# Optimization experiments

Hardware: AMD Instinct MI355X
Metric: run time of the kernel (lower is better)

The kernel has to match this reference:

```python
import jax, jax.numpy as jnp
import numpy as np

IN_FEATURES = 512
OUT_FEATURES = 512
GRID_MIN = -2.0
GRID_MAX = 2.0
NUM_GRIDS = 8
SPLINE_SCALE = 0.1
BATCH = 16384


def setup_inputs() -> dict:
    key = jax.random.key(0)
    kx, kw = jax.random.split(key)
    x = jax.random.normal(kx, (BATCH, IN_FEATURES), dtype=jnp.float32)
    grid = jnp.linspace(GRID_MIN, GRID_MAX, NUM_GRIDS, dtype=jnp.float32)
    spline_weight = (
        jax.random.normal(kw, (IN_FEATURES * NUM_GRIDS, OUT_FEATURES), dtype=jnp.float32)
        * SPLINE_SCALE
    )
    return {"x": x, "grid": grid, "spline_weight": spline_weight}


def reference(x, grid, spline_weight):
    # denominator h = (grid_max - grid_min) / (num_grids - 1)
    h = (GRID_MAX - GRID_MIN) / (NUM_GRIDS - 1)
    # basis: [B, in_features, num_grids]
    basis = jnp.exp(-jnp.square((x[..., None] - grid) / h))
    # flatten to [B, in_features * num_grids] and GEMM
    return basis.reshape(basis.shape[0], -1) @ spline_weight
```

## Files before the change

### kernel.cpp

```cpp
#include <hip/hip_runtime.h>
#include <hip/hip_bf16.h>

#define BATCH 16384
#define IN_F 512
#define OUT_F 512
#define NG 8
#define KTOT (IN_F * NG)

#define SH    2.1019642153762872f
#define SSTEP 1.2011224087864498f
#define BC0N  4.2039284307525745f
#define RC1   2.4022448175728996f
#define RC2  -1.4426950408889634f
#define RQ    0.13533528323661270f

typedef __attribute__((ext_vector_type(8))) short short8;
typedef __attribute__((ext_vector_type(4))) float f32x4;
typedef __attribute__((ext_vector_type(2))) float f32x2;
typedef __attribute__((ext_vector_type(4))) unsigned int u32x4;
typedef __attribute__((ext_vector_type(2))) unsigned int u32x2;

__device__ __forceinline__ unsigned fbits(float f) {
    union { float f; unsigned u; } v; v.f = f; return v.u;
}
__device__ __forceinline__ unsigned pack2bf(float lo, float hi) {
    unsigned a = (fbits(lo) + 0x8000u) >> 16;
    unsigned b = (fbits(hi) + 0x8000u) & 0xFFFF0000u;
    return a | b;
}

__device__ __forceinline__ void lds_barrier() {
    __asm__ volatile("" ::: "memory");
    __builtin_amdgcn_sched_barrier(0);
    __builtin_amdgcn_s_waitcnt(0xC07F);
    __builtin_amdgcn_s_barrier();
    __builtin_amdgcn_sched_barrier(0);
    __asm__ volatile("" ::: "memory");
}

__global__ void wt_swizzle(const float* __restrict__ W, unsigned short* __restrict__ Wt) {
    const int gid  = blockIdx.x * 256 + threadIdx.x;
    const int lane = gid & 63;
    const int f    = (gid >> 6) & 7;
    const int kt   = (gid >> 9) & 63;
    const int s    = gid >> 15;
    const int j  = f & 3, kk = f >> 2;
    const int l15 = lane & 15, lq = lane >> 4;
    const int n  = s * 64 + j * 16 + l15;
    const int k0 = kt * 64 + kk * 32 + lq * 8;
    u32x4 pk;
#pragma unroll
    for (int e = 0; e < 4; ++e)
        pk[e] = pack2bf(W[(size_t)(k0 + 2 * e) * OUT_F + n],
                        W[(size_t)(k0 + 2 * e + 1) * OUT_F + n]);
    *(u32x4*)(Wt + (size_t)gid * 8) = pk;
}

__global__ __launch_bounds__(256, 2) void gauss_gemm5(
        const float* __restrict__ X, const unsigned short* __restrict__ Wt,
        float* __restrict__ Out) {
    __shared__ __align__(16) unsigned short sA[2 * 64 * 64];

    const int tid  = threadIdx.x;
    const int lane = tid & 63;
    const int wave = tid >> 6;
    const int cb = blockIdx.x & 1;
    const int rb = blockIdx.x >> 1;
    const int m0 = rb * 64;
    const int n0 = cb * 256;
    const int l15 = lane & 15;
    const int lq  = lane >> 4;
    const int s   = cb * 4 + wave;

    const int aw0 = lane * 64 + (((2 * wave)     ^ (lane & 7)) << 3);
    const int aw1 = lane * 64 + (((2 * wave + 1) ^ (lane & 7)) << 3);
    const float* xlp = X + (size_t)(m0 + lane) * IN_F + wave * 2;

    int aofs[2][4];
#pragma unroll
    for (int kk = 0; kk < 2; ++kk)
#pragma unroll
        for (int i = 0; i < 4; ++i)
            aofs[kk][i] = (i * 16 + l15) * 64 + (((kk * 4 + lq) ^ (l15 & 7)) << 3);

    const unsigned short* bptr = Wt + (size_t)s * 262144 + lane * 8;

    f32x4 acc[4][4];
#pragma unroll
    for (int i = 0; i < 4; ++i)
#pragma unroll
        for (int j = 0; j < 4; ++j)
            acc[i][j] = (f32x4){0.f, 0.f, 0.f, 0.f};

    auto stageA = [&](f32x2 xv, int buf) {
        unsigned short* base = sA + buf * 4096;
#pragma unroll
        for (int h = 0; h < 2; ++h) {
            const float t0 = fmaf(h ? xv.y : xv.x, SH, BC0N);
            float r = __builtin_amdgcn_exp2f(fmaf(t0, RC1, RC2));
            const float v0 = __builtin_amdgcn_exp2f(-t0 * t0);
            const float v1 = v0 * r;
            r *= RQ; const float v2 = v1 * r;
            r *= RQ; const float v3 = v2 * r;
            r *= RQ; const float v4 = v3 * r;
            r *= RQ; const float v5 = v4 * r;
            r *= RQ; const float v6 = v5 * r;
            r *= RQ; const float v7 = v6 * r;
            u32x4 pk;
            pk[0] = pack2bf(v0, v1);
            pk[1] = pack2bf(v2, v3);
            pk[2] = pack2bf(v4, v5);
            pk[3] = pack2bf(v6, v7);
            *(u32x4*)(base + (h ? aw1 : aw0)) = pk;
        }
    };

    short8 bfA[8], bfB[8];
    f32x2 xr;

    {
        f32x2 x0 = *(const f32x2*)(xlp);
        stageA(x0, 0);
#pragma unroll
        for (int f = 0; f < 8; ++f)
            bfA[f] = *(const short8*)(bptr + f * 512);
        xr = *(const f32x2*)(xlp + 8);
        lds_barrier();
    }

#define GG_ITER(KT, BUF, BU, BF)                                               \
    {                                                                          \
        const int kn1 = ((KT) + 1 < 63) ? (KT) + 1 : 63;                       \
        const int kn2 = ((KT) + 2 < 63) ? (KT) + 2 : 63;                       \
        short8 af[2][4];                                                       \
        _Pragma("unroll")                                                      \
        for (int kk = 0; kk < 2; ++kk)                                         \
            _Pragma("unroll")                                                  \
            for (int i = 0; i < 4; ++i)                                        \
                af[kk][i] = *(const short8*)(sA + (BUF) * 4096 + aofs[kk][i]); \
        _Pragma("unroll")                                                      \
        for (int f = 0; f < 8; ++f)                                            \
            BF[f] = *(const short8*)(bptr + (size_t)kn1 * 4096 + f * 512);     \
        stageA(xr, (BUF) ^ 1);                                                 \
        xr = *(const f32x2*)(xlp + (size_t)kn2 * 8);                           \
        _Pragma("unroll")                                                      \
        for (int kk = 0; kk < 2; ++kk)                                         \
            _Pragma("unroll")                                                  \
            for (int i = 0; i < 4; ++i)                                        \
                _Pragma("unroll")                                              \
                for (int j = 0; j < 4; ++j)                                    \
                    acc[i][j] = __builtin_amdgcn_mfma_f32_16x16x32_bf16(       \
                        af[kk][i], BU[kk * 4 + j], acc[i][j], 0, 0, 0);        \
        lds_barrier();                                                         \
    }

    for (int kt = 0; kt < 64; kt += 2) {
        GG_ITER(kt,     0, bfA, bfB)
        GG_ITER(kt + 1, 1, bfB, bfA)
    }
#undef GG_ITER

#pragma unroll
    for (int i = 0; i < 4; ++i) {
        const int r0 = m0 + i * 16 + lq * 4;
#pragma unroll
        for (int j = 0; j < 4; ++j) {
            const int c = n0 + wave * 64 + j * 16 + l15;
#pragma unroll
            for (int e = 0; e < 4; ++e)
                Out[(size_t)(r0 + e) * OUT_F + c] = acc[i][j][e];
        }
    }
}

#define BM 128
#define BN 128
#define BK 64
#define LDA 72
#define LDB 72

__global__ __launch_bounds__(256, 2) void gauss_gemm_fb(
        const float* __restrict__ X, const float* __restrict__ W,
        float* __restrict__ Out) {
    __shared__ __align__(16) unsigned short sA[BM * LDA];
    __shared__ __align__(16) unsigned short sB2[BN * LDB];

    const int tid  = threadIdx.x;
    const int lane = tid & 63;
    const int wave = tid >> 6;
    const int rb = blockIdx.x >> 2;
    const int cbx = blockIdx.x & 3;
    const int m0 = rb * BM;
    const int n0 = cbx * BN;
    const int wr = (wave >> 1) * 64;
    const int wc = (wave & 1) * 64;
    const int l15 = lane & 15;
    const int lq  = lane >> 4;

    f32x4 acc[4][4];
#pragma unroll
    for (int i = 0; i < 4; ++i)
#pragma unroll
        for (int j = 0; j < 4; ++j)
            acc[i][j] = (f32x4){0.f, 0.f, 0.f, 0.f};

    const int arow = tid & 127;
    const int axq  = tid >> 7;

    for (int kt = 0; kt < KTOT / BK; ++kt) {
        const int k0  = kt * BK;
        const int xc0 = kt * (BK / NG);

        const f32x4 xv = *(const f32x4*)(X + (size_t)(m0 + arow) * IN_F + xc0 + 4 * axq);
        unsigned short* sArow = sA + arow * LDA + axq * 32;
#pragma unroll
        for (int j = 0; j < 4; ++j) {
            const float xs = xv[j] * SH;
            u32x4 pk;
#pragma unroll
            for (int g = 0; g < 8; g += 2) {
                float t0 = xs + (BC0N - g * SSTEP);
                float t1 = xs + (BC0N - (g + 1) * SSTEP);
                unsigned u0 = fbits(__builtin_amdgcn_exp2f(-t0 * t0)) + 0x8000u;
                unsigned u1 = fbits(__builtin_amdgcn_exp2f(-t1 * t1)) + 0x8000u;
                pk[g >> 1] = (u0 >> 16) | (u1 & 0xFFFF0000u);
            }
            *(u32x4*)(sArow + j * 8) = pk;
        }

#pragma unroll
        for (int p = 0; p < 8; ++p) {
            int id = p * 256 + tid;
            int n  = id & 127;
            int k4 = id >> 7;
            const float* wp = W + (size_t)(k0 + k4 * 4) * OUT_F + n0 + n;
            u32x2 v;
            v[0] = pack2bf(wp[0], wp[OUT_F]);
            v[1] = pack2bf(wp[2 * OUT_F], wp[3 * OUT_F]);
            *(u32x2*)(sB2 + n * LDB + k4 * 4) = v;
        }

        __syncthreads();

#pragma unroll
        for (int kk = 0; kk < BK; kk += 32) {
            short8 af[4], bfv[4];
#pragma unroll
            for (int i = 0; i < 4; ++i)
                af[i] = *(const short8*)(sA + (wr + i * 16 + l15) * LDA + kk + lq * 8);
#pragma unroll
            for (int i = 0; i < 4; ++i)
                bfv[i] = *(const short8*)(sB2 + (wc + i * 16 + l15) * LDB + kk + lq * 8);
#pragma unroll
            for (int i = 0; i < 4; ++i)
#pragma unroll
                for (int j = 0; j < 4; ++j)
                    acc[i][j] = __builtin_amdgcn_mfma_f32_16x16x32_bf16(af[i], bfv[j], acc[i][j], 0, 0, 0);
        }

        __syncthreads();
    }

#pragma unroll
    for (int i = 0; i < 4; ++i) {
        const int r0 = m0 + wr + i * 16 + lq * 4;
#pragma unroll
        for (int j = 0; j < 4; ++j) {
            const int c = n0 + wc + j * 16 + l15;
#pragma unroll
            for (int e = 0; e < 4; ++e)
                Out[(size_t)(r0 + e) * OUT_F + c] = acc[i][j][e];
        }
    }
}

extern "C" void kernel_launch(void* const* d_in, const int* in_sizes, int n_in,
                              void* d_out, int out_size, void* d_ws, size_t ws_size,
                              hipStream_t stream) {
    (void)in_sizes; (void)n_in; (void)out_size;
    const float* X = (const float*)d_in[0];
    const float* W = (const float*)d_in[2];
    float* Out = (float*)d_out;

    const size_t wt_bytes = (size_t)KTOT * OUT_F * sizeof(unsigned short);
    if (ws_size >= wt_bytes) {
        unsigned short* Wt = (unsigned short*)d_ws;
        wt_swizzle<<<dim3(KTOT * OUT_F / 8 / 256), 256, 0, stream>>>(W, Wt);
        gauss_gemm5<<<dim3((BATCH / 64) * (OUT_F / 256)), 256, 0, stream>>>(X, Wt, Out);
    } else {
        gauss_gemm_fb<<<dim3((BATCH / BM) * (OUT_F / BN)), 256, 0, stream>>>(X, W, Out);
    }
}
```

Baseline: 156.2 us.

## Compute Gaussian basis directly in MFMA A-fragment registers, drop LDS staging

```diff
diff --git a/kernel.cpp b/kernel.cpp
--- a/kernel.cpp
+++ b/kernel.cpp
@@ -27,15 +27,6 @@
     unsigned a = (fbits(lo) + 0x8000u) >> 16;
     unsigned b = (fbits(hi) + 0x8000u) & 0xFFFF0000u;
     return a | b;
-}
-
-__device__ __forceinline__ void lds_barrier() {
-    __asm__ volatile("" ::: "memory");
-    __builtin_amdgcn_sched_barrier(0);
-    __builtin_amdgcn_s_waitcnt(0xC07F);
-    __builtin_amdgcn_s_barrier();
-    __builtin_amdgcn_sched_barrier(0);
-    __asm__ volatile("" ::: "memory");
 }
 
 __global__ void wt_swizzle(const float* __restrict__ W, unsigned short* __restrict__ Wt) {
@@ -47,7 +38,7 @@
     const int j  = f & 3, kk = f >> 2;
     const int l15 = lane & 15, lq = lane >> 4;
     const int n  = s * 64 + j * 16 + l15;
-    const int k0 = kt * 64 + kk * 32 + lq * 8;
+    const int k0 = kt * 64 + (lq * 2 + kk) * 8;
     u32x4 pk;
 #pragma unroll
     for (int e = 0; e < 4; ++e)
@@ -56,11 +47,9 @@
     *(u32x4*)(Wt + (size_t)gid * 8) = pk;
 }
 
-__global__ __launch_bounds__(256, 2) void gauss_gemm5(
+__global__ __launch_bounds__(256, 2) void gauss_gemm6(
         const float* __restrict__ X, const unsigned short* __restrict__ Wt,
         float* __restrict__ Out) {
-    __shared__ __align__(16) unsigned short sA[2 * 64 * 64];
-
     const int tid  = threadIdx.x;
     const int lane = tid & 63;
     const int wave = tid >> 6;
@@ -72,18 +61,12 @@
     const int lq  = lane >> 4;
     const int s   = cb * 4 + wave;
 
-    const int aw0 = lane * 64 + (((2 * wave)     ^ (lane & 7)) << 3);
-    const int aw1 = lane * 64 + (((2 * wave + 1) ^ (lane & 7)) << 3);
-    const float* xlp = X + (size_t)(m0 + lane) * IN_F + wave * 2;
-
-    int aofs[2][4];
-#pragma unroll
-    for (int kk = 0; kk < 2; ++kk)
-#pragma unroll
-        for (int i = 0; i < 4; ++i)
-            aofs[kk][i] = (i * 16 + l15) * 64 + (((kk * 4 + lq) ^ (l15 & 7)) << 3);
-
     const unsigned short* bptr = Wt + (size_t)s * 262144 + lane * 8;
+
+    const float* xrow[4];
+#pragma unroll
+    for (int i = 0; i < 4; ++i)
+        xrow[i] = X + (size_t)(m0 + i * 16 + l15) * IN_F + lq * 2;
 
     f32x4 acc[4][4];
 #pragma unroll
@@ -92,71 +75,62 @@
         for (int j = 0; j < 4; ++j)
             acc[i][j] = (f32x4){0.f, 0.f, 0.f, 0.f};
 
-    auto stageA = [&](f32x2 xv, int buf) {
-        unsigned short* base = sA + buf * 4096;
-#pragma unroll
-        for (int h = 0; h < 2; ++h) {
-            const float t0 = fmaf(h ? xv.y : xv.x, SH, BC0N);
-            float r = __builtin_amdgcn_exp2f(fmaf(t0, RC1, RC2));
-            const float v0 = __builtin_amdgcn_exp2f(-t0 * t0);
-            const float v1 = v0 * r;
-            r *= RQ; const float v2 = v1 * r;
-            r *= RQ; const float v3 = v2 * r;
-            r *= RQ; const float v4 = v3 * r;
-            r *= RQ; const float v5 = v4 * r;
-            r *= RQ; const float v6 = v5 * r;
-            r *= RQ; const float v7 = v6 * r;
-            u32x4 pk;
-            pk[0] = pack2bf(v0, v1);
-            pk[1] = pack2bf(v2, v3);
-            pk[2] = pack2bf(v4, v5);
-            pk[3] = pack2bf(v6, v7);
-            *(u32x4*)(base + (h ? aw1 : aw0)) = pk;
-        }
+    short8 bc[8], bn[8];
+    f32x2 xc[4], xn[4];
+
+#pragma unroll
+    for (int f = 0; f < 8; ++f)
+        bc[f] = *(const short8*)(bptr + f * 512);
+#pragma unroll
+    for (int i = 0; i < 4; ++i)
+        xc[i] = *(const f32x2*)(xrow[i]);
+
+    auto gauss8 = [&](float x) -> short8 {
+        const float t0 = fmaf(x, SH, BC0N);
+        float r = __builtin_amdgcn_exp2f(fmaf(t0, RC1, RC2));
+        const float v0 = __builtin_amdgcn_exp2f(-t0 * t0);
+        const float v1 = v0 * r;
+        r *= RQ; const float v2 = v1 * r;
+        r *= RQ; const float v3 = v2 * r;
+        r *= RQ; const float v4 = v3 * r;
+        r *= RQ; const float v5 = v4 * r;
+        r *= RQ; const float v6 = v5 * r;
+        r *= RQ; const float v7 = v6 * r;
+        u32x4 pk;
+        pk[0] = pack2bf(v0, v1);
+        pk[1] = pack2bf(v2, v3);
+        pk[2] = pack2bf(v4, v5);
+        pk[3] = pack2bf(v6, v7);
+        return *(short8*)&pk;
     };
 
-    short8 bfA[8], bfB[8];
-    f32x2 xr;
-
-    {
-        f32x2 x0 = *(const f32x2*)(xlp);
-        stageA(x0, 0);
-#pragma unroll
-        for (int f = 0; f < 8; ++f)
-            bfA[f] = *(const short8*)(bptr + f * 512);
-        xr = *(const f32x2*)(xlp + 8);
-        lds_barrier();
-    }
-
-#define GG_ITER(KT, BUF, BU, BF)                                               \
+#define GG_ITER(KT, BC_, BN_, XC_, XN_)                                        \
     {                                                                          \
         const int kn1 = ((KT) + 1 < 63) ? (KT) + 1 : 63;                       \
-        const int kn2 = ((KT) + 2 < 63) ? (KT) + 2 : 63;                       \
-        short8 af[2][4];                                                       \
         _Pragma("unroll")                                                      \
-        for (int kk = 0; kk < 2; ++kk)                                         \
+        for (int f = 0; f < 8; ++f)                                            \
+            BN_[f] = *(const short8*)(bptr + (size_t)kn1 * 4096 + f * 512);    \
+        _Pragma("unroll")                                                      \
+        for (int i = 0; i < 4; ++i)                                            \
+            XN_[i] = *(const f32x2*)(xrow[i] + (size_t)kn1 * 8);               \
+        _Pragma("unroll")                                                      \
+        for (int kk = 0; kk < 2; ++kk) {                                       \
+            short8 af[4];                                                      \
             _Pragma("unroll")                                                  \
             for (int i = 0; i < 4; ++i)                                        \
-                af[kk][i] = *(const short8*)(sA + (BUF) * 4096 + aofs[kk][i]); \
-        _Pragma("unroll")                                                      \
-        for (int f = 0; f < 8; ++f)                                            \
-            BF[f] = *(const short8*)(bptr + (size_t)kn1 * 4096 + f * 512);     \
-        stageA(xr, (BUF) ^ 1);                                                 \
-        xr = *(const f32x2*)(xlp + (size_t)kn2 * 8);                           \
-        _Pragma("unroll")                                                      \
-        for (int kk = 0; kk < 2; ++kk)                                         \
+                af[i] = gauss8(kk ? XC_[i].y : XC_[i].x);                      \
             _Pragma("unroll")                                                  \
             for (int i = 0; i < 4; ++i)                                        \
                 _Pragma("unroll")                                              \
                 for (int j = 0; j < 4; ++j)                                    \
                     acc[i][j] = __builtin_amdgcn_mfma_f32_16x16x32_bf16(       \
-                        af[kk][i], BU[kk * 4 + j], acc[i][j], 0, 0, 0);        \
-        lds_barrier();                                                         \
+                        af[i], BC_[kk * 4 + j], acc[i][j], 0, 0, 0);           \
+        }                                                                      \
     }
 
     for (int kt = 0; kt < 64; kt += 2) {
-        GG_ITER(kt,     0, bfA, bfB)
-        GG_ITER(kt + 1, 1, bfB, bfA)
+        GG_ITER(kt,     bc, bn, xc, xn)
+        GG_ITER(kt + 1, bn, bc, xn, xc)
     }
 #undef GG_ITER
 
@@ -286,7 +260,7 @@
     if (ws_size >= wt_bytes) {
         unsigned short* Wt = (unsigned short*)d_ws;
         wt_swizzle<<<dim3(KTOT * OUT_F / 8 / 256), 256, 0, stream>>>(W, Wt);
-        gauss_gemm5<<<dim3((BATCH / 64) * (OUT_F / 256)), 256, 0, stream>>>(X, Wt, Out);
+        gauss_gemm6<<<dim3((BATCH / 64) * (OUT_F / 256)), 256, 0, stream>>>(X, Wt, Out);
     } else {
         gauss_gemm_fb<<<dim3((BATCH / BM) * (OUT_F / BN)), 256, 0, stream>>>(X, W, Out);
     }
```

New measurement: 217.1 us. +39.0%, slower.
